# Performance work log

Hardware: AMD Instinct MI355X
Metric: run time of the kernel (lower is better)

## Reference

```python
import jax, jax.numpy as jnp
import numpy as np

D_MODEL = 2048
N_HEADS = 32
N_KV_HEADS = 8
HEAD_DIM = D_MODEL // N_HEADS          # 64
GROUP = N_HEADS // N_KV_HEADS          # 4
B, T = 1, 2048
SWA_WINDOW = 512


def _rope_tables(T, half_dim):
    # standard RoPE frequencies, theta=10000
    inv_freq = 1.0 / (10000.0 ** (np.arange(half_dim, dtype=np.float32) / half_dim))
    pos = np.arange(T, dtype=np.float32)
    ang = pos[:, None] * inv_freq[None, :]          # [T, D/2]
    return jnp.asarray(np.sin(ang)), jnp.asarray(np.cos(ang))


def setup_inputs() -> dict:
    key = jax.random.key(0)
    ks = jax.random.split(key, 5)
    scale = 1.0 / np.sqrt(D_MODEL)
    x = jax.random.normal(ks[0], (B, T, D_MODEL), dtype=jnp.float32)
    Wq = jax.random.normal(ks[1], (D_MODEL, N_HEADS * HEAD_DIM), dtype=jnp.float32) * scale
    Wk = jax.random.normal(ks[2], (D_MODEL, N_KV_HEADS * HEAD_DIM), dtype=jnp.float32) * scale
    Wv = jax.random.normal(ks[3], (D_MODEL, N_KV_HEADS * HEAD_DIM), dtype=jnp.float32) * scale
    Wo = jax.random.normal(ks[4], (N_HEADS * HEAD_DIM, D_MODEL), dtype=jnp.float32) * scale
    rope_sin, rope_cos = _rope_tables(T, HEAD_DIM // 2)
    return {"x": x, "Wq": Wq, "Wk": Wk, "Wv": Wv, "Wo": Wo,
            "rope_sin": rope_sin, "rope_cos": rope_cos, "swa_window": SWA_WINDOW}


def apply_rope(x, sin, cos):
    # x: [B, T, H, D]; sin/cos: [T, D/2], interleaved-pair rotation in fp32
    orig_dtype = x.dtype
    Bx, Tx, Hx, Dx = x.shape
    xf = x.astype(jnp.float32).reshape(Bx, Tx, Hx, Dx // 2, 2)
    x1, x2 = xf[..., 0], xf[..., 1]
    s = sin.astype(jnp.float32)[None, :, None, :]
    c = cos.astype(jnp.float32)[None, :, None, :]
    out = jnp.stack((x1 * c - x2 * s, x1 * s + x2 * c), axis=-1)
    return out.reshape(Bx, Tx, Hx, Dx).astype(orig_dtype)


def reference(x, Wq, Wk, Wv, Wo, rope_sin, rope_cos, swa_window):
    Bx, Tx, C = x.shape
    q = (x @ Wq).reshape(Bx, Tx, N_HEADS, HEAD_DIM)
    k = (x @ Wk).reshape(Bx, Tx, N_KV_HEADS, HEAD_DIM)
    v = (x @ Wv).reshape(Bx, Tx, N_KV_HEADS, HEAD_DIM)

    q = apply_rope(q, rope_sin, rope_cos)
    k = apply_rope(k, rope_sin, rope_cos)

    # repeat_interleave KV heads to match query heads (GQA)
    k = jnp.repeat(k, GROUP, axis=2)   # [B, T, H, D]
    v = jnp.repeat(v, GROUP, axis=2)

    q = q.transpose(0, 2, 1, 3)        # [B, H, T, D]
    k = k.transpose(0, 2, 1, 3)
    v = v.transpose(0, 2, 1, 3)

    # causal + sliding-window mask: disallow j > i or i - j > swa_window
    idx = jnp.arange(Tx)
    delta = idx[:, None] - idx[None, :]          # [T, T], i - j
    disallowed = delta < 0
    if swa_window > 0:
        disallowed = disallowed | (delta > swa_window)

    scale = 1.0 / np.sqrt(HEAD_DIM)
    scores = jnp.einsum('bhqd,bhkd->bhqk', q, k) * scale
    scores = jnp.where(disallowed[None, None], -jnp.inf, scores)
    weights = jax.nn.softmax(scores, axis=-1)
    attn = jnp.einsum('bhqk,bhkd->bhqd', weights, v)   # [B, H, T, D]

    attn = attn.transpose(0, 2, 1, 3).reshape(Bx, Tx, C)
    return attn @ Wo
```

## Files before the change

kernel.cpp:

```cpp
#include <hip/hip_runtime.h>
#include <math.h>

#define DMODEL 2048
#define NH     32
#define NKV    8
#define HDIM   64
#define GROUP  4
#define KVW    (NKV * HDIM)

typedef short bf16x8 __attribute__((ext_vector_type(8)));
typedef float f32x4  __attribute__((ext_vector_type(4)));

__device__ __forceinline__ short f2bf(float f) {
    union { float f; unsigned u; } x; x.f = f;
    unsigned r = x.u + 0x7fffu + ((x.u >> 16) & 1u);
    return (short)(r >> 16);
}
__device__ __forceinline__ float bf2f(short h) {
    union { unsigned u; float f; } x; x.u = ((unsigned)(unsigned short)h) << 16;
    return x.f;
}

typedef __attribute__((address_space(3))) void lds_void;
typedef const __attribute__((address_space(1))) void gbl_void;
__device__ __forceinline__ void gll16(const void* g, void* l) {
    __builtin_amdgcn_global_load_lds((gbl_void*)g, (lds_void*)l, 16, 0, 0);
}

__global__ __launch_bounds__(256)
void split_f32(const float* __restrict__ in, short* __restrict__ oh,
               short* __restrict__ ol, int n4)
{
    int i = blockIdx.x * 256 + threadIdx.x;
    if (i >= n4) return;
    float4 v = ((const float4*)in)[i];
    short h0 = f2bf(v.x), h1 = f2bf(v.y), h2 = f2bf(v.z), h3 = f2bf(v.w);
    short l0 = f2bf(v.x - bf2f(h0)), l1 = f2bf(v.y - bf2f(h1));
    short l2 = f2bf(v.z - bf2f(h2)), l3 = f2bf(v.w - bf2f(h3));
    ((short4*)oh)[i] = make_short4(h0, h1, h2, h3);
    ((short4*)ol)[i] = make_short4(l0, l1, l2, l3);
}

__global__ __launch_bounds__(256)
void transpose_split_f32(const float* __restrict__ W, int K, int N,
                         short* __restrict__ oth, short* __restrict__ otl, int ldo)
{
    __shared__ float tile[32][33];
    const int bx = blockIdx.x, by = blockIdx.y;
    const int c = threadIdx.x & 31, r = threadIdx.x >> 5;
    #pragma unroll
    for (int it = 0; it < 4; ++it)
        tile[r + it * 8][c] = W[(size_t)(by * 32 + r + it * 8) * N + bx * 32 + c];
    __syncthreads();
    #pragma unroll
    for (int it = 0; it < 4; ++it) {
        int n = bx * 32 + r + it * 8;
        int k = by * 32 + c;
        float v = tile[c][r + it * 8];
        short h = f2bf(v), l = f2bf(v - bf2f(h));
        oth[(size_t)n * ldo + k] = h;
        otl[(size_t)n * ldo + k] = l;
    }
}

__global__ __launch_bounds__(256)
void transpose_bf16(const short* __restrict__ in, int R, int C,
                    short* __restrict__ out)
{
    __shared__ short tile[32][33];
    const int bx = blockIdx.x, by = blockIdx.y;
    const int c = threadIdx.x & 31, r = threadIdx.x >> 5;
    #pragma unroll
    for (int it = 0; it < 4; ++it)
        tile[r + it * 8][c] = in[(size_t)(by * 32 + r + it * 8) * C + bx * 32 + c];
    __syncthreads();
    #pragma unroll
    for (int it = 0; it < 4; ++it)
        out[(size_t)(bx * 32 + r + it * 8) * R + by * 32 + c] = tile[c][r + it * 8];
}

template <int MODE>
__global__ __launch_bounds__(256)
void gemm3(const short* __restrict__ Ah, const short* __restrict__ Al,
           const short* __restrict__ Bh, const short* __restrict__ Bl,
           int K,
           float* __restrict__ C, int ldc,
           short* __restrict__ Qo, short* __restrict__ Ko, short* __restrict__ Vo,
           const float* __restrict__ rs, const float* __restrict__ rc)
{
    __shared__ __align__(16) short AhS[2][128 * 32];
    __shared__ __align__(16) short AlS[2][128 * 32];
    __shared__ __align__(16) short BhS[2][128 * 32];
    __shared__ __align__(16) short BlS[2][128 * 32];

    const int t = threadIdx.x, lane = t & 63, w = t >> 6;
    const int wr = (w >> 1) * 64, wc = (w & 1) * 64;
    const int m0 = blockIdx.y * 128, n0 = blockIdx.x * 128;

    f32x4 zero = {0.f, 0.f, 0.f, 0.f};
    f32x4 acc[4][4];
    #pragma unroll
    for (int i = 0; i < 4; ++i)
        #pragma unroll
        for (int j = 0; j < 4; ++j) acc[i][j] = zero;

    const int sr0 = (w * 2 + 0) * 16 + (lane >> 2);
    const int sr1 = (w * 2 + 1) * 16 + (lane >> 2);
    const int sc0 = (((lane & 3) ^ (sr0 & 3)) * 8);
    const int sc1 = (((lane & 3) ^ (sr1 & 3)) * 8);
    const size_t ga0 = (size_t)(m0 + sr0) * K + sc0;
    const size_t ga1 = (size_t)(m0 + sr1) * K + sc1;
    const size_t gb0 = (size_t)(n0 + sr0) * K + sc0;
    const size_t gb1 = (size_t)(n0 + sr1) * K + sc1;
    const int co0 = (w * 2 + 0) * 1024;
    const int co1 = (w * 2 + 1) * 1024;

    const int fr = lane & 15, fs = lane >> 4;

    auto stage = [&](int k0, int p) {
        gll16(Ah + ga0 + k0, (char*)AhS[p] + co0);
        gll16(Ah + ga1 + k0, (char*)AhS[p] + co1);
        gll16(Al + ga0 + k0, (char*)AlS[p] + co0);
        gll16(Al + ga1 + k0, (char*)AlS[p] + co1);
        gll16(Bh + gb0 + k0, (char*)BhS[p] + co0);
        gll16(Bh + gb1 + k0, (char*)BhS[p] + co1);
        gll16(Bl + gb0 + k0, (char*)BlS[p] + co0);
        gll16(Bl + gb1 + k0, (char*)BlS[p] + co1);
    };

    const int nsteps = K >> 5;
    stage(0, 0);

    for (int s = 0; s < nsteps; ++s) {
        const int p = s & 1;
        __syncthreads();
        if (s + 1 < nsteps) stage((s + 1) << 5, p ^ 1);

        bf16x8 fah[4], fal[4], fbh[4], fbl[4];
        #pragma unroll
        for (int i = 0; i < 4; ++i) {
            int ar = wr + i * 16 + fr;
            int aoff = ar * 64 + ((fs ^ (ar & 3)) << 4);
            fah[i] = *(const bf16x8*)((const char*)AhS[p] + aoff);
            fal[i] = *(const bf16x8*)((const char*)AlS[p] + aoff);
            int br = wc + i * 16 + fr;
            int boff = br * 64 + ((fs ^ (br & 3)) << 4);
            fbh[i] = *(const bf16x8*)((const char*)BhS[p] + boff);
            fbl[i] = *(const bf16x8*)((const char*)BlS[p] + boff);
        }
        #pragma unroll
        for (int i = 0; i < 4; ++i)
            #pragma unroll
            for (int j = 0; j < 4; ++j) {
                acc[i][j] = __builtin_amdgcn_mfma_f32_16x16x32_bf16(fah[i], fbh[j], acc[i][j], 0, 0, 0);
                acc[i][j] = __builtin_amdgcn_mfma_f32_16x16x32_bf16(fah[i], fbl[j], acc[i][j], 0, 0, 0);
                acc[i][j] = __builtin_amdgcn_mfma_f32_16x16x32_bf16(fal[i], fbh[j], acc[i][j], 0, 0, 0);
            }
    }

    const int g = lane >> 4;
    #pragma unroll
    for (int i = 0; i < 4; ++i)
        #pragma unroll
        for (int j = 0; j < 4; ++j)
            #pragma unroll
            for (int r = 0; r < 4; ++r) {
                int m = m0 + wr + i * 16 + g * 4 + r;
                int n = n0 + wc + j * 16 + fr;
                float v = acc[i][j][r];
                if (MODE == 0) {
                    C[(size_t)m * ldc + n] = v;
                } else {
                    if (n < 2048 + 512) {
                        float pp = __shfl_xor(v, 1);
                        int pi = (n & (HDIM - 1)) >> 1;
                        float sn = rs[m * (HDIM / 2) + pi];
                        float cs = rc[m * (HDIM / 2) + pi];
                        v = ((lane & 1) == 0) ? (v * cs - pp * sn) : (pp * sn + v * cs);
                    }
                    short b = f2bf(v);
                    if (n < 2048)            Qo[(size_t)m * DMODEL + n] = b;
                    else if (n < 2048 + 512) Ko[(size_t)m * KVW + (n - 2048)] = b;
                    else                     Vo[(size_t)m * KVW + (n - 2560)] = b;
                }
            }
}

__global__ __launch_bounds__(256)
void attn_mfma(const short* __restrict__ Qb, const short* __restrict__ Kb,
               const short* __restrict__ Vt, short* __restrict__ AoH,
               short* __restrict__ AoL, const int* __restrict__ swa_ptr, int T)
{
    __shared__ __align__(16) short Ks[2][32 * 64];
    __shared__ __align__(16) short Vs[2][64 * 32];
    __shared__ __align__(16) short Ps[4][16 * 32];

    const int h = blockIdx.y, qt = blockIdx.x;
    const int q0 = qt * 64, hk = h >> 2;
    const int t = threadIdx.x, lane = t & 63, w = t >> 6;
    const int swa = *swa_ptr;
    const int fr = lane & 15, g = lane >> 4;
    const int qrow = q0 + w * 16;

    bf16x8 qf0, qf1;
    {
        const short* qp = Qb + (size_t)(qrow + fr) * DMODEL + h * HDIM + g * 8;
        qf0 = *(const bf16x8*)qp;
        qf1 = *(const bf16x8*)(qp + 32);
    }

    f32x4 zero = {0.f, 0.f, 0.f, 0.f};
    f32x4 oacc[4];
    #pragma unroll
    for (int dt = 0; dt < 4; ++dt) oacc[dt] = zero;
    float mreg[4] = {-INFINITY, -INFINITY, -INFINITY, -INFINITY};
    float lreg[4] = {0.f, 0.f, 0.f, 0.f};

    int kt_lo = 0;
    if (swa > 0) { int lo = q0 - swa; if (lo > 0) kt_lo = lo >> 5; }
    const int kt_hi = (q0 + 63) >> 5;

    const int krow = w * 8 + (lane >> 3);
    const int kcol = (((lane & 7) ^ (krow & 7)) * 8);
    const size_t kgbase = (size_t)krow * KVW + hk * HDIM + kcol;
    const int vrow = w * 16 + (lane >> 2);
    const int vcol = (((lane & 3) ^ (vrow & 3)) * 8);
    const size_t vgbase = (size_t)(hk * HDIM + vrow) * T + vcol;

    auto stage = [&](int kt, int p) {
        gll16(Kb + (size_t)(kt * 32) * KVW + kgbase, (char*)Ks[p] + w * 1024);
        gll16(Vt + vgbase + kt * 32, (char*)Vs[p] + w * 1024);
    };

    stage(kt_lo, 0);

    for (int kt = kt_lo; kt <= kt_hi; ++kt) {
        const int k0 = kt * 32;
        const int p = (kt - kt_lo) & 1;
        __syncthreads();
        if (kt + 1 <= kt_hi) stage(kt + 1, p ^ 1);

        f32x4 s0a = zero, s1a = zero;
        #pragma unroll
        for (int ks = 0; ks < 2; ++ks) {
            int slot = g + ks * 4;
            int key0 = fr, key1 = 16 + fr;
            bf16x8 kf0 = *(const bf16x8*)((const char*)Ks[p] + key0 * 128 + ((slot ^ (key0 & 7)) << 4));
            bf16x8 kf1 = *(const bf16x8*)((const char*)Ks[p] + key1 * 128 + ((slot ^ (key1 & 7)) << 4));
            bf16x8 qf = ks ? qf1 : qf0;
            s0a = __builtin_amdgcn_mfma_f32_16x16x32_bf16(qf, kf0, s0a, 0, 0, 0);
            s1a = __builtin_amdgcn_mfma_f32_16x16x32_bf16(qf, kf1, s1a, 0, 0, 0);
        }

        const bool full = (k0 + 31 <= qrow) && (swa <= 0 || (qrow + 15 - k0) <= swa);

        float alpha[4], p0v[4], p1v[4];
        #pragma unroll
        for (int r = 0; r < 4; ++r) {
            float s0, s1;
            if (full) {
                s0 = s0a[r] * 0.125f;
                s1 = s1a[r] * 0.125f;
            } else {
                int i = qrow + g * 4 + r;
                int j0 = k0 + fr, j1 = k0 + 16 + fr;
                int d0 = i - j0, d1 = i - j1;
                s0 = (d0 >= 0 && (swa <= 0 || d0 <= swa)) ? s0a[r] * 0.125f : -INFINITY;
                s1 = (d1 >= 0 && (swa <= 0 || d1 <= swa)) ? s1a[r] * 0.125f : -INFINITY;
            }
            float rm = fmaxf(s0, s1);
            rm = fmaxf(rm, __shfl_xor(rm, 1));
            rm = fmaxf(rm, __shfl_xor(rm, 2));
            rm = fmaxf(rm, __shfl_xor(rm, 4));
            rm = fmaxf(rm, __shfl_xor(rm, 8));
            float mo = mreg[r];
            float mn = fmaxf(mo, rm);
            float a, p0, p1;
            if (mn == -INFINITY) { a = 1.f; p0 = 0.f; p1 = 0.f; }
            else {
                a  = __expf(mo - mn);
                p0 = __expf(s0 - mn);
                p1 = __expf(s1 - mn);
            }
            float rsum = p0 + p1;
            rsum += __shfl_xor(rsum, 1);
            rsum += __shfl_xor(rsum, 2);
            rsum += __shfl_xor(rsum, 4);
            rsum += __shfl_xor(rsum, 8);
            mreg[r] = mn;
            lreg[r] = lreg[r] * a + rsum;
            alpha[r] = a;
            p0v[r] = p0;
            p1v[r] = p1;
        }

        #pragma unroll
        for (int r = 0; r < 4; ++r) {
            int row = g * 4 + r;
            int c0 = fr, c1 = 16 + fr;
            *(short*)((char*)Ps[w] + row * 64 + (((c0 >> 3) ^ (row & 3)) << 4) + ((c0 & 7) << 1)) = f2bf(p0v[r]);
            *(short*)((char*)Ps[w] + row * 64 + (((c1 >> 3) ^ (row & 3)) << 4) + ((c1 & 7) << 1)) = f2bf(p1v[r]);
        }

        #pragma unroll
        for (int dt = 0; dt < 4; ++dt)
            #pragma unroll
            for (int r = 0; r < 4; ++r) oacc[dt][r] = oacc[dt][r] * alpha[r];

        {
            int prow = fr;
            bf16x8 pf = *(const bf16x8*)((const char*)Ps[w] + prow * 64 + ((g ^ (prow & 3)) << 4));
            #pragma unroll
            for (int dt = 0; dt < 4; ++dt) {
                int d = dt * 16 + fr;
                bf16x8 vf = *(const bf16x8*)((const char*)Vs[p] + d * 64 + ((g ^ (d & 3)) << 4));
                oacc[dt] = __builtin_amdgcn_mfma_f32_16x16x32_bf16(pf, vf, oacc[dt], 0, 0, 0);
            }
        }
    }

    float invl[4];
    #pragma unroll
    for (int r = 0; r < 4; ++r) invl[r] = 1.0f / lreg[r];
    #pragma unroll
    for (int dt = 0; dt < 4; ++dt)
        #pragma unroll
        for (int r = 0; r < 4; ++r) {
            int i = qrow + g * 4 + r;
            float v = oacc[dt][r] * invl[r];
            int col = h * HDIM + dt * 16 + fr;
            short hb = f2bf(v);
            short lb = f2bf(v - bf2f(hb));
            AoH[(size_t)i * DMODEL + col] = hb;
            AoL[(size_t)i * DMODEL + col] = lb;
        }
}

extern "C" void kernel_launch(void* const* d_in, const int* in_sizes, int n_in,
                              void* d_out, int out_size, void* d_ws, size_t ws_size,
                              hipStream_t stream)
{
    const float* x    = (const float*)d_in[0];
    const float* Wq   = (const float*)d_in[1];
    const float* Wk   = (const float*)d_in[2];
    const float* Wv   = (const float*)d_in[3];
    const float* Wo   = (const float*)d_in[4];
    const float* rsin = (const float*)d_in[5];
    const float* rcos = (const float*)d_in[6];
    const int*   swa  = (const int*)d_in[7];

    const int T = in_sizes[0] / DMODEL;

    char* p = (char*)d_ws;
    short* WTh  = (short*)p; p += (size_t)3072 * 2048 * 2;
    short* WTl  = (short*)p; p += (size_t)3072 * 2048 * 2;
    short* WoTh = (short*)p; p += (size_t)2048 * 2048 * 2;
    short* WoTl = (short*)p; p += (size_t)2048 * 2048 * 2;
    short* Xh   = (short*)p; p += (size_t)T * DMODEL * 2;
    short* Xl   = (short*)p; p += (size_t)T * DMODEL * 2;
    short* Qbf  = (short*)p; p += (size_t)T * DMODEL * 2;
    short* Kbf  = (short*)p; p += (size_t)T * KVW * 2;
    short* Vbf  = (short*)p; p += (size_t)T * KVW * 2;
    short* Vt   = (short*)p; p += (size_t)T * KVW * 2;
    short* AoH  = Xh;
    short* AoL  = Xl;

    int n4 = T * DMODEL / 4;
    split_f32<<<(n4 + 255) / 256, 256, 0, stream>>>(x, Xh, Xl, n4);

    transpose_split_f32<<<dim3(2048 / 32, 2048 / 32), 256, 0, stream>>>(Wq, 2048, 2048, WTh, WTl, 2048);
    transpose_split_f32<<<dim3(512 / 32, 2048 / 32), 256, 0, stream>>>(Wk, 2048, 512, WTh + (size_t)2048 * 2048, WTl + (size_t)2048 * 2048, 2048);
    transpose_split_f32<<<dim3(512 / 32, 2048 / 32), 256, 0, stream>>>(Wv, 2048, 512, WTh + (size_t)2560 * 2048, WTl + (size_t)2560 * 2048, 2048);
    transpose_split_f32<<<dim3(2048 / 32, 2048 / 32), 256, 0, stream>>>(Wo, 2048, 2048, WoTh, WoTl, 2048);

    gemm3<1><<<dim3(3072 / 128, T / 128), 256, 0, stream>>>(
        Xh, Xl, WTh, WTl, 2048, nullptr, 0, Qbf, Kbf, Vbf, rsin, rcos);

    transpose_bf16<<<dim3(KVW / 32, T / 32), 256, 0, stream>>>(Vbf, T, KVW, Vt);

    attn_mfma<<<dim3(T / 64, NH), 256, 0, stream>>>(Qbf, Kbf, Vt, AoH, AoL, swa, T);

    gemm3<0><<<dim3(2048 / 128, T / 128), 256, 0, stream>>>(
        AoH, AoL, WoTh, WoTl, 2048, (float*)d_out, 2048, nullptr, nullptr, nullptr, nullptr, nullptr);
}
```

Measured before the change: 354.3 us.

## Split-K GEMMs into two halves with separate reduce kernels, add MFMA priority hints

Both projection GEMMs now run split-K with two K halves as a grid z dimension. Partial fp32 results go to a workspace, and separate reduce kernels sum them and apply RoPE and the bf16 conversion for QKV. The GEMM drops LDS double buffering in favour of a single buffer with two barriers per step, which halves LDS use and may raise occupancy, and changes the swizzle pattern. s_setprio hints are added around the attention MFMAs. The changes add partial-sum write and read traffic plus two extra launches, and the single-buffered loop loses load/compute overlap.

```diff
diff --git a/kernel.cpp b/kernel.cpp
--- a/kernel.cpp
+++ b/kernel.cpp
@@ -79,23 +79,21 @@
         out[(size_t)(bx * 32 + r + it * 8) * R + by * 32 + c] = tile[c][r + it * 8];
 }
 
-template <int MODE>
-__global__ __launch_bounds__(256)
-void gemm3(const short* __restrict__ Ah, const short* __restrict__ Al,
-           const short* __restrict__ Bh, const short* __restrict__ Bl,
-           int K,
-           float* __restrict__ C, int ldc,
-           short* __restrict__ Qo, short* __restrict__ Ko, short* __restrict__ Vo,
-           const float* __restrict__ rs, const float* __restrict__ rc)
-{
-    __shared__ __align__(16) short AhS[2][128 * 32];
-    __shared__ __align__(16) short AlS[2][128 * 32];
-    __shared__ __align__(16) short BhS[2][128 * 32];
-    __shared__ __align__(16) short BlS[2][128 * 32];
+__global__ __launch_bounds__(256)
+void gemm3s(const short* __restrict__ Ah, const short* __restrict__ Al,
+            const short* __restrict__ Bh, const short* __restrict__ Bl,
+            int K, int ldc, float* __restrict__ P)
+{
+    __shared__ __align__(16) short AhS[128 * 32];
+    __shared__ __align__(16) short AlS[128 * 32];
+    __shared__ __align__(16) short BhS[128 * 32];
+    __shared__ __align__(16) short BlS[128 * 32];
 
     const int t = threadIdx.x, lane = t & 63, w = t >> 6;
     const int wr = (w >> 1) * 64, wc = (w & 1) * 64;
     const int m0 = blockIdx.y * 128, n0 = blockIdx.x * 128;
+    const int kbase = blockIdx.z * (K >> 1);
+    float* out = P + (size_t)blockIdx.z * ((size_t)gridDim.y * 128) * ldc;
 
     f32x4 zero = {0.f, 0.f, 0.f, 0.f};
     f32x4 acc[4][4];
@@ -106,47 +104,42 @@
 
     const int sr0 = (w * 2 + 0) * 16 + (lane >> 2);
     const int sr1 = (w * 2 + 1) * 16 + (lane >> 2);
-    const int sc0 = (((lane & 3) ^ (sr0 & 3)) * 8);
-    const int sc1 = (((lane & 3) ^ (sr1 & 3)) * 8);
-    const size_t ga0 = (size_t)(m0 + sr0) * K + sc0;
-    const size_t ga1 = (size_t)(m0 + sr1) * K + sc1;
-    const size_t gb0 = (size_t)(n0 + sr0) * K + sc0;
-    const size_t gb1 = (size_t)(n0 + sr1) * K + sc1;
+    const int sc0 = (((lane & 3) ^ ((sr0 >> 1) & 3)) * 8);
+    const int sc1 = (((lane & 3) ^ ((sr1 >> 1) & 3)) * 8);
+    const size_t ga0 = (size_t)(m0 + sr0) * K + kbase + sc0;
+    const size_t ga1 = (size_t)(m0 + sr1) * K + kbase + sc1;
+    const size_t gb0 = (size_t)(n0 + sr0) * K + kbase + sc0;
+    const size_t gb1 = (size_t)(n0 + sr1) * K + kbase + sc1;
     const int co0 = (w * 2 + 0) * 1024;
     const int co1 = (w * 2 + 1) * 1024;
 
     const int fr = lane & 15, fs = lane >> 4;
 
-    auto stage = [&](int k0, int p) {
-        gll16(Ah + ga0 + k0, (char*)AhS[p] + co0);
-        gll16(Ah + ga1 + k0, (char*)AhS[p] + co1);
-        gll16(Al + ga0 + k0, (char*)AlS[p] + co0);
-        gll16(Al + ga1 + k0, (char*)AlS[p] + co1);
-        gll16(Bh + gb0 + k0, (char*)BhS[p] + co0);
-        gll16(Bh + gb1 + k0, (char*)BhS[p] + co1);
-        gll16(Bl + gb0 + k0, (char*)BlS[p] + co0);
-        gll16(Bl + gb1 + k0, (char*)BlS[p] + co1);
-    };
-
-    const int nsteps = K >> 5;
-    stage(0, 0);
-
+    const int nsteps = K >> 6;
     for (int s = 0; s < nsteps; ++s) {
-        const int p = s & 1;
+        const int k0 = s << 5;
         __syncthreads();
-        if (s + 1 < nsteps) stage((s + 1) << 5, p ^ 1);
+        gll16(Ah + ga0 + k0, (char*)AhS + co0);
+        gll16(Ah + ga1 + k0, (char*)AhS + co1);
+        gll16(Al + ga0 + k0, (char*)AlS + co0);
+        gll16(Al + ga1 + k0, (char*)AlS + co1);
+        gll16(Bh + gb0 + k0, (char*)BhS + co0);
+        gll16(Bh + gb1 + k0, (char*)BhS + co1);
+        gll16(Bl + gb0 + k0, (char*)BlS + co0);
+        gll16(Bl + gb1 + k0, (char*)BlS + co1);
+        __syncthreads();
 
         bf16x8 fah[4], fal[4], fbh[4], fbl[4];
         #pragma unroll
         for (int i = 0; i < 4; ++i) {
             int ar = wr + i * 16 + fr;
-            int aoff = ar * 64 + ((fs ^ (ar & 3)) << 4);
-            fah[i] = *(const bf16x8*)((const char*)AhS[p] + aoff);
-            fal[i] = *(const bf16x8*)((const char*)AlS[p] + aoff);
+            int aoff = ar * 64 + ((fs ^ ((ar >> 1) & 3)) << 4);
+            fah[i] = *(const bf16x8*)((const char*)AhS + aoff);
+            fal[i] = *(const bf16x8*)((const char*)AlS + aoff);
             int br = wc + i * 16 + fr;
-            int boff = br * 64 + ((fs ^ (br & 3)) << 4);
-            fbh[i] = *(const bf16x8*)((const char*)BhS[p] + boff);
-            fbl[i] = *(const bf16x8*)((const char*)BlS[p] + boff);
+            int boff = br * 64 + ((fs ^ ((br >> 1) & 3)) << 4);
+            fbh[i] = *(const bf16x8*)((const char*)BhS + boff);
+            fbl[i] = *(const bf16x8*)((const char*)BlS + boff);
         }
         #pragma unroll
         for (int i = 0; i < 4; ++i)
@@ -167,23 +160,64 @@
             for (int r = 0; r < 4; ++r) {
                 int m = m0 + wr + i * 16 + g * 4 + r;
                 int n = n0 + wc + j * 16 + fr;
-                float v = acc[i][j][r];
-                if (MODE == 0) {
-                    C[(size_t)m * ldc + n] = v;
-                } else {
-                    if (n < 2048 + 512) {
-                        float pp = __shfl_xor(v, 1);
-                        int pi = (n & (HDIM - 1)) >> 1;
-                        float sn = rs[m * (HDIM / 2) + pi];
-                        float cs = rc[m * (HDIM / 2) + pi];
-                        v = ((lane & 1) == 0) ? (v * cs - pp * sn) : (pp * sn + v * cs);
-                    }
-                    short b = f2bf(v);
-                    if (n < 2048)            Qo[(size_t)m * DMODEL + n] = b;
-                    else if (n < 2048 + 512) Ko[(size_t)m * KVW + (n - 2048)] = b;
-                    else                     Vo[(size_t)m * KVW + (n - 2560)] = b;
-                }
+                out[(size_t)m * ldc + n] = acc[i][j][r];
             }
+}
+
+__global__ __launch_bounds__(256)
+void reduce_qkv(const float* __restrict__ P,
+                const float* __restrict__ rs, const float* __restrict__ rc,
+                short* __restrict__ Qo, short* __restrict__ Ko,
+                short* __restrict__ Vo)
+{
+    const int idx = blockIdx.x * 256 + threadIdx.x;
+    const int row = idx / 384;
+    const int c8  = (idx - row * 384) * 8;
+    const float* p0 = P + (size_t)row * 3072 + c8;
+    const float* p1 = p0 + (size_t)2048 * 3072;
+    float4 a0 = *(const float4*)p0,       a1 = *(const float4*)(p0 + 4);
+    float4 b0 = *(const float4*)p1,       b1 = *(const float4*)(p1 + 4);
+    float v[8] = {a0.x + b0.x, a0.y + b0.y, a0.z + b0.z, a0.w + b0.w,
+                  a1.x + b1.x, a1.y + b1.y, a1.z + b1.z, a1.w + b1.w};
+    if (c8 < 2560) {
+        int pib = (c8 & 63) >> 1;
+        #pragma unroll
+        for (int j = 0; j < 4; ++j) {
+            float sn = rs[row * (HDIM / 2) + pib + j];
+            float cs = rc[row * (HDIM / 2) + pib + j];
+            float e = v[2 * j], o = v[2 * j + 1];
+            v[2 * j]     = e * cs - o * sn;
+            v[2 * j + 1] = e * sn + o * cs;
+        }
+    }
+    short s[8];
+    #pragma unroll
+    for (int j = 0; j < 8; ++j) s[j] = f2bf(v[j]);
+    short4 lo = make_short4(s[0], s[1], s[2], s[3]);
+    short4 hi = make_short4(s[4], s[5], s[6], s[7]);
+    if (c8 < 2048) {
+        short* q = Qo + (size_t)row * DMODEL + c8;
+        *(short4*)q = lo; *(short4*)(q + 4) = hi;
+    } else if (c8 < 2560) {
+        short* k = Ko + (size_t)row * KVW + (c8 - 2048);
+        *(short4*)k = lo; *(short4*)(k + 4) = hi;
+    } else {
+        short* vv = Vo + (size_t)row * KVW + (c8 - 2560);
+        *(short4*)vv = lo; *(short4*)(vv + 4) = hi;
+    }
+}
+
+__global__ __launch_bounds__(256)
+void reduce_out(const float* __restrict__ P, float* __restrict__ out)
+{
+    const int i = (blockIdx.x * 256 + threadIdx.x) * 8;
+    const float* p1 = P + (size_t)2048 * 2048;
+    float4 a0 = *(const float4*)(P + i),  a1 = *(const float4*)(P + i + 4);
+    float4 b0 = *(const float4*)(p1 + i), b1 = *(const float4*)(p1 + i + 4);
+    float4 o0 = make_float4(a0.x + b0.x, a0.y + b0.y, a0.z + b0.z, a0.w + b0.w);
+    float4 o1 = make_float4(a1.x + b1.x, a1.y + b1.y, a1.z + b1.z, a1.w + b1.w);
+    *(float4*)(out + i) = o0;
+    *(float4*)(out + i + 4) = o1;
 }
 
 __global__ __launch_bounds__(256)
@@ -241,6 +275,7 @@
         if (kt + 1 <= kt_hi) stage(kt + 1, p ^ 1);
 
         f32x4 s0a = zero, s1a = zero;
+        __builtin_amdgcn_s_setprio(1);
         #pragma unroll
         for (int ks = 0; ks < 2; ++ks) {
             int slot = g + ks * 4;
@@ -251,6 +286,7 @@
             s0a = __builtin_amdgcn_mfma_f32_16x16x32_bf16(qf, kf0, s0a, 0, 0, 0);
             s1a = __builtin_amdgcn_mfma_f32_16x16x32_bf16(qf, kf1, s1a, 0, 0, 0);
         }
+        __builtin_amdgcn_s_setprio(0);
 
         const bool full = (k0 + 31 <= qrow) && (swa <= 0 || (qrow + 15 - k0) <= swa);
 
@@ -310,12 +346,14 @@
         {
             int prow = fr;
             bf16x8 pf = *(const bf16x8*)((const char*)Ps[w] + prow * 64 + ((g ^ (prow & 3)) << 4));
+            __builtin_amdgcn_s_setprio(1);
             #pragma unroll
             for (int dt = 0; dt < 4; ++dt) {
                 int d = dt * 16 + fr;
                 bf16x8 vf = *(const bf16x8*)((const char*)Vs[p] + d * 64 + ((g ^ (d & 3)) << 4));
                 oacc[dt] = __builtin_amdgcn_mfma_f32_16x16x32_bf16(pf, vf, oacc[dt], 0, 0, 0);
             }
+            __builtin_amdgcn_s_setprio(0);
         }
     }
 
@@ -362,6 +400,7 @@
     short* Kbf  = (short*)p; p += (size_t)T * KVW * 2;
     short* Vbf  = (short*)p; p += (size_t)T * KVW * 2;
     short* Vt   = (short*)p; p += (size_t)T * KVW * 2;
+    float* Part = (float*)p; p += (size_t)2 * T * 3072 * 4;
     short* AoH  = Xh;
     short* AoL  = Xl;
 
@@ -373,13 +412,15 @@
     transpose_split_f32<<<dim3(512 / 32, 2048 / 32), 256, 0, stream>>>(Wv, 2048, 512, WTh + (size_t)2560 * 2048, WTl + (size_t)2560 * 2048, 2048);
     transpose_split_f32<<<dim3(2048 / 32, 2048 / 32), 256, 0, stream>>>(Wo, 2048, 2048, WoTh, WoTl, 2048);
 
-    gemm3<1><<<dim3(3072 / 128, T / 128), 256, 0, stream>>>(
-        Xh, Xl, WTh, WTl, 2048, nullptr, 0, Qbf, Kbf, Vbf, rsin, rcos);
+    gemm3s<<<dim3(3072 / 128, T / 128, 2), 256, 0, stream>>>(
+        Xh, Xl, WTh, WTl, 2048, 3072, Part);
+    reduce_qkv<<<T * 3072 / 8 / 256, 256, 0, stream>>>(Part, rsin, rcos, Qbf, Kbf, Vbf);
 
     transpose_bf16<<<dim3(KVW / 32, T / 32), 256, 0, stream>>>(Vbf, T, KVW, Vt);
 
     attn_mfma<<<dim3(T / 64, NH), 256, 0, stream>>>(Qbf, Kbf, Vt, AoH, AoL, swa, T);
 
-    gemm3<0><<<dim3(2048 / 128, T / 128), 256, 0, stream>>>(
-        AoH, AoL, WoTh, WoTl, 2048, (float*)d_out, 2048, nullptr, nullptr, nullptr, nullptr, nullptr);
-}
+    gemm3s<<<dim3(2048 / 128, T / 128, 2), 256, 0, stream>>>(
+        AoH, AoL, WoTh, WoTl, 2048, 2048, Part);
+    reduce_out<<<T * 2048 / 8 / 256, 256, 0, stream>>>(Part, (float*)d_out);
+}
```

New measurement: 322.2 us. 1.1x faster.
